# Optimization experiments

Hardware: AMD Instinct MI355X
Metric: run time of the kernel (lower is better)

The kernel has to match this reference:

```python
import jax, jax.numpy as jnp
import numpy as np

MIN_NORM = 1e-15
BALL_EPS = 4e-3          # float32 boundary eps (HGCN convention), c = 1
RES_LAMBDA = 0.5         # args.res_lambda (global in original repo)
N_HOPS = 2


def _artanh(x):
    x = jnp.clip(x, -1.0 + 1e-7, 1.0 - 1e-7)
    return 0.5 * jnp.log((1.0 + x) / (1.0 - x))


def _norm(x):
    return jnp.clip(jnp.linalg.norm(x, axis=-1, keepdims=True), MIN_NORM, None)


def expmap0(u):
    n = _norm(u)
    return jnp.tanh(n) * u / n


def mobius_add(x, y):
    x2 = jnp.sum(x * x, axis=-1, keepdims=True)
    y2 = jnp.sum(y * y, axis=-1, keepdims=True)
    xy = jnp.sum(x * y, axis=-1, keepdims=True)
    num = (1.0 + 2.0 * xy + y2) * x + (1.0 - x2) * y
    den = jnp.clip(1.0 + 2.0 * xy + x2 * y2, MIN_NORM, None)
    return num / den


def expmap(u, p):
    lam = 2.0 / jnp.clip(1.0 - jnp.sum(p * p, axis=-1, keepdims=True), MIN_NORM, None)
    n = _norm(u)
    second = jnp.tanh(0.5 * lam * n) * u / n
    return mobius_add(p, second)


def logmap(y, p):
    sub = mobius_add(-p, y)
    n = _norm(sub)
    lam = 2.0 / jnp.clip(1.0 - jnp.sum(p * p, axis=-1, keepdims=True), MIN_NORM, None)
    return (2.0 / lam) * _artanh(n) * sub / n


def project(x):
    n = _norm(x)
    maxnorm = 1.0 - BALL_EPS
    return jnp.where(n > maxnorm, x / n * maxnorm, x)


def _l2_normalize(x, eps=1e-12):
    return x / jnp.clip(jnp.linalg.norm(x, axis=-1, keepdims=True), eps, None)


def setup_inputs() -> dict:
    key = jax.random.key(0)
    k1, k2, k3, k4, k5 = jax.random.split(key, 5)
    n_entities, n_relations, latdim, n_edges = 200000, 32, 64, 1000000
    entity_emb = 0.1 * jax.random.normal(k1, (n_entities, latdim), dtype=jnp.float32)
    relation_emb = 0.1 * jax.random.normal(k2, (n_relations, latdim), dtype=jnp.float32)
    head = jax.random.randint(k3, (n_edges,), 0, n_entities)
    tail = jax.random.randint(k4, (n_edges,), 0, n_entities)
    edge_index = jnp.stack([head, tail], axis=0).astype(jnp.int64)
    edge_type = jax.random.randint(k5, (n_edges,), 1, n_relations + 1).astype(jnp.int64)
    return {"entity_emb": entity_emb, "relation_emb": relation_emb,
            "edge_index": edge_index, "edge_type": edge_type}


def _agg(entity_emb, relation_emb, head, tail, relation_type):
    n_entities = entity_emb.shape[0]
    head_emb = entity_emb[head]            # [E, d]
    tail_emb = entity_emb[tail]            # [E, d]
    rel_emb = relation_emb[relation_type]  # [E, d]
    ricci = _l2_normalize(tail_emb + rel_emb)
    hyper_head = expmap0(head_emb)
    hyper_tail = expmap(tail_emb, hyper_head)
    hyper_rel = expmap(rel_emb, hyper_head)
    res = project(mobius_add(hyper_tail, hyper_rel))
    res = logmap(res, hyper_head) + ricci * 1e-7
    res = jax.nn.relu(res)
    # scatter_mean by head index
    sums = jnp.zeros((n_entities, res.shape[-1]), res.dtype).at[head].add(res)
    counts = jnp.zeros((n_entities,), res.dtype).at[head].add(1.0)
    return sums / jnp.clip(counts, 1.0, None)[:, None]


def reference(entity_emb, relation_emb, edge_index, edge_type):
    head, tail = edge_index[0], edge_index[1]
    relation_type = edge_type - 1
    entity_res_emb = entity_emb
    e = entity_emb
    for _ in range(N_HOPS):
        e = _agg(e, relation_emb, head, tail, relation_type)
        e = _l2_normalize(e)  # F.normalize (dropout disabled for determinism)
        entity_res_emb = RES_LAMBDA * entity_res_emb + e
    return entity_res_emb
```

## Files before the change

### kernel.cpp

```cpp
#include <hip/hip_runtime.h>
#include <cmath>

#define MIN_NORM 1e-15f
#define RCPF(x)  __builtin_amdgcn_rcpf(x)
#define SQRTF(x) __builtin_amdgcn_sqrtf(x)
#define RSQF(x)  __builtin_amdgcn_rsqf(x)

template<int CTRL>
__device__ __forceinline__ float dpp_add(float v) {
    return __int_as_float(__builtin_amdgcn_update_dpp(0, __float_as_int(v), CTRL, 0xF, 0xF, false));
}

__device__ __forceinline__ float rsum16(float v) {
    v += dpp_add<0x121>(v);
    v += dpp_add<0x122>(v);
    v += dpp_add<0x124>(v);
    v += dpp_add<0x128>(v);
    return v;
}

__device__ __forceinline__ float rsum8(float v) {
    v += dpp_add<0xB1>(v);
    v += dpp_add<0x4E>(v);
    v += dpp_add<0x141>(v);
    return v;
}

__device__ __forceinline__ float tanh_fast(float x) {
    float ex = __expf(fminf(2.f * x, 30.f));
    return (ex - 1.f) * RCPF(ex + 1.f);
}

__global__ __launch_bounds__(256) void k_pass1(
    const int*    __restrict__ head,
    const float4* __restrict__ ent,
    const float4* __restrict__ rel,
    int*    __restrict__ C,
    float2* __restrict__ Th1,
    float2* __restrict__ Tt1,
    float2* __restrict__ RelC1,
    float2* __restrict__ RelC2,
    float ILAM2, int E, int N, int NR, int EB, int PG)
{
    int b = (int)blockIdx.x;
    if (b < EB) {
        int i = b * 256 + (int)threadIdx.x;
        if (i < E) atomicAdd(&C[head[i]], 1);
    } else if (b < EB + PG) {
        int gid = ((b - EB) * 256 + (int)threadIdx.x) >> 4;
        int g   = (int)threadIdx.x & 15;
        if (gid >= N) return;
        float4 v = ent[(size_t)gid * 16 + g];
        float n2 = rsum16(v.x * v.x + v.y * v.y + v.z * v.z + v.w * v.w);
        if (g == 0) {
            float nh     = fmaxf(SQRTF(fmaxf(n2, 0.f)), MIN_NORM);
            float inv_nh = RCPF(nh);
            float th     = tanh_fast(nh);
            Th1[gid] = make_float2(th * inv_nh, th * th);
            Tt1[gid] = make_float2(nh, inv_nh);
        }
    } else {
        int gid = ((b - EB - PG) * 256 + (int)threadIdx.x) >> 4;
        int g   = (int)threadIdx.x & 15;
        if (gid >= NR) return;
        float4 v = rel[(size_t)gid * 16 + g];
        float n2 = rsum16(v.x * v.x + v.y * v.y + v.z * v.z + v.w * v.w);
        if (g == 0) {
            float nr = fmaxf(SQRTF(n2), MIN_NORM);
            float inv_nr = RCPF(nr);
            RelC1[gid] = make_float2(nr, inv_nr);
            float thr2 = tanh_fast(ILAM2 * nr);
            RelC2[gid] = make_float2(thr2 * inv_nr, thr2 * thr2);
        }
    }
}

__global__ __launch_bounds__(256) void k_scan1(const int* __restrict__ C,
                                               int* __restrict__ T,
                                               int* __restrict__ BS,
                                               int* __restrict__ DH, int N) {
    __shared__ int lds[256];
    __shared__ int lh[64];
    if (threadIdx.x < 64) lh[threadIdx.x] = 0;
    int i = blockIdx.x * 256 + (int)threadIdx.x;
    int v = (i < N) ? C[i] : 0;
    lds[threadIdx.x] = v;
    __syncthreads();
    for (int off = 1; off < 256; off <<= 1) {
        int add = (threadIdx.x >= (unsigned)off) ? lds[threadIdx.x - off] : 0;
        __syncthreads();
        lds[threadIdx.x] += add;
        __syncthreads();
    }
    if (i < N) {
        T[i] = lds[threadIdx.x];
        int bd = 63 - min(v, 63);
        atomicAdd(&lh[bd], 1);
    }
    if (threadIdx.x == 255) BS[blockIdx.x] = lds[255];
    __syncthreads();
    if (threadIdx.x < 64 && lh[threadIdx.x] > 0)
        atomicAdd(&DH[threadIdx.x], lh[threadIdx.x]);
}

__global__ __launch_bounds__(1024) void k_scan2(int* __restrict__ BS,
                                                const int* __restrict__ DH,
                                                int* __restrict__ DB, int nb) {
    if (blockIdx.x == 0) {
        __shared__ int lds[1024];
        int v = ((int)threadIdx.x < nb) ? BS[threadIdx.x] : 0;
        lds[threadIdx.x] = v;
        __syncthreads();
        for (int off = 1; off < 1024; off <<= 1) {
            int add = (threadIdx.x >= (unsigned)off) ? lds[threadIdx.x - off] : 0;
            __syncthreads();
            lds[threadIdx.x] += add;
            __syncthreads();
        }
        if ((int)threadIdx.x < nb) BS[threadIdx.x] = lds[threadIdx.x] - v;
    } else {
        __shared__ int lds[64];
        if (threadIdx.x >= 64) return;
        int t = (int)threadIdx.x;
        int v = DH[t];
        lds[t] = v;
        __syncthreads();
        for (int off = 1; off < 64; off <<= 1) {
            int add = (t >= off) ? lds[t - off] : 0;
            __syncthreads();
            lds[t] += add;
            __syncthreads();
        }
        DB[t] = lds[t] - v;
    }
}

__global__ __launch_bounds__(256) void k_scan3(const int* __restrict__ C,
                                               const int* __restrict__ T,
                                               const int* __restrict__ BS,
                                               int2* __restrict__ OC,
                                               int* __restrict__ P, int N) {
    int i = blockIdx.x * 256 + (int)threadIdx.x;
    if (i < N) {
        int c = C[i];
        int beg = T[i] - c + BS[blockIdx.x];
        OC[i] = make_int2(beg, c);
        P[i] = beg;
    }
}

__global__ __launch_bounds__(256) void k_pass2(
    const int* __restrict__ C,
    int*       __restrict__ DB,
    int*       __restrict__ perm,
    const int* __restrict__ head,
    const int* __restrict__ tail,
    const int* __restrict__ etype,
    int*       __restrict__ P,
    int*       __restrict__ rec,
    int N, int E, int NB, int SLICES)
{
    int b = (int)blockIdx.x;
    if (b < NB) {
        __shared__ int lh[64];
        __shared__ int lbase[64];
        if (threadIdx.x < 64) lh[threadIdx.x] = 0;
        __syncthreads();
        int i = b * 256 + (int)threadIdx.x;
        int bd = -1, lr = 0;
        if (i < N) {
            bd = 63 - min(C[i], 63);
            lr = atomicAdd(&lh[bd], 1);
        }
        __syncthreads();
        if (threadIdx.x < 64 && lh[threadIdx.x] > 0)
            lbase[threadIdx.x] = atomicAdd(&DB[threadIdx.x], lh[threadIdx.x]);
        __syncthreads();
        if (bd >= 0) perm[lbase[bd] + lr] = i;
    } else {
        int region = b & 7;
        int slice  = (b - NB) >> 3;
        int rlo = (int)(((long long)region * N) >> 3);
        int rhi = (int)(((long long)(region + 1) * N) >> 3);
        int step = 256 * SLICES;
        for (int i = slice * 256 + (int)threadIdx.x; i < E; i += step) {
            int h = head[i];
            int t = tail[i];
            int et = etype[i];
            if (h >= rlo && h < rhi) {
                int pos = atomicAdd(&P[h], 1);
                rec[pos] = t | ((et - 1) << 20);
            }
        }
    }
}

template<bool HOP2>
__global__ __launch_bounds__(256) void rgat_hop_kernel(
    const float*  __restrict__ e,
    const float*  __restrict__ rel,
    const float2* __restrict__ Th1,
    const float2* __restrict__ Tt1,
    const float2* __restrict__ Tt2,
    const float2* __restrict__ RelC1,
    const float2* __restrict__ RelC2,
    const int*    __restrict__ rec,
    const int2*   __restrict__ OC,
    const int*    __restrict__ perm,
    const float*  __restrict__ ent,
    float*        __restrict__ dst0,
    float2*       __restrict__ Tt2w,
    float SCP2, float P2C, float ILAM2, int N)
{
    int tid  = blockIdx.x * 256 + (int)threadIdx.x;
    int slot = tid >> 3;
    int l    = (int)threadIdx.x & 7;
    bool act = slot < N;
    int h    = perm[act ? slot : 0];

    int2 oc = OC[h];
    int beg = act ? oc.x : 0;
    int end = act ? (oc.x + oc.y) : 0;

    const float* hrow = e + (size_t)h * 64 + l;
    float hv[8];
#pragma unroll
    for (int k = 0; k < 8; ++k) hv[k] = hrow[8 * k];

    float scp, p2;
    if constexpr (HOP2) {
        scp = SCP2; p2 = P2C;
    } else {
        float2 th = Th1[h];
        scp = th.x; p2 = th.y;
    }
    float bet  = fmaxf(1.f - p2, MIN_NORM);
    float ilam = RCPF(bet);
    float bet2 = bet * bet;

    float acc[8];
#pragma unroll
    for (int k = 0; k < 8; ++k) acc[k] = 0.f;

    float tA[8], rA[8], tB[8], rB[8];
    float2 tvA, rvA, tvB, rvB;

    auto LD = [&](int i, float* T, float* R, float2& TV, float2& RV) {
        int rc = rec[i];
        int ti = rc & 0xFFFFF;
        int ri = rc >> 20;
        const float* tr = e   + (size_t)ti * 64 + l;
        const float* rr = rel + (size_t)ri * 64 + l;
#pragma unroll
        for (int k = 0; k < 8; ++k) { T[k] = tr[8 * k]; R[k] = rr[8 * k]; }
        if constexpr (HOP2) { TV = Tt2[ti]; RV = RelC2[ri]; }
        else               { TV = Tt1[ti]; RV = RelC1[ri]; }
    };

    auto COMPUTE = [&](const float* t, const float* r, float2 tv, float2 rv) {
        float pht = 0.f, phr = 0.f, ptr_ = 0.f;
#pragma unroll
        for (int k = 0; k < 8; ++k) {
            pht  += hv[k] * t[k];
            phr  += hv[k] * r[k];
            ptr_ += t[k] * r[k];
        }
        float ht  = rsum8(pht);
        float hr  = rsum8(phr);
        float ttr = rsum8(ptr_);

        float sct, y2t, scr, y2r;
        if constexpr (HOP2) {
            sct = tv.x; y2t = tv.y;
            scr = rv.x; y2r = rv.y;
        } else {
            float tht = tanh_fast(ilam * tv.x);
            sct = tht * tv.y;  y2t = tht * tht;
            float thr_ = tanh_fast(ilam * rv.x);
            scr = thr_ * rv.y; y2r = thr_ * thr_;
        }

        float xyt = scp * sct * ht;
        float xyr = scp * scr * hr;

        float alt  = fmaf(2.f, xyt, 1.f + y2t);
        float dent = fmaxf(fmaf(p2, y2t, fmaf(2.f, xyt, 1.f)), MIN_NORM);
        float alr  = fmaf(2.f, xyr, 1.f + y2r);
        float denr = fmaxf(fmaf(p2, y2r, fmaf(2.f, xyr, 1.f)), MIN_NORM);
        float iS   = RCPF(dent * denr);
        float idt  = iS * denr;
        float idr  = iS * dent;

        float a2 = (alt * alt * p2 + 2.f * alt * bet * xyt + bet * bet * y2t) * idt * idt;
        float pa = fmaf(bet, xyt, alt * p2) * idt;
        float b2 = (alr * alr * p2 + 2.f * alr * bet * xyr + bet * bet * y2r) * idr * idr;
        float pb = fmaf(bet, xyr, alr * p2) * idr;

        float ytyr = sct * scr * ttr;
        float ab = (alt * alr * p2 + alt * bet * xyr + bet * alr * xyt + bet * bet * ytyr) * idt * idr;

        float am   = fmaf(2.f, ab, 1.f + b2);
        float bm   = 1.f - a2;
        float denm = fmaxf(fmaf(a2, b2, fmaf(2.f, ab, 1.f)), MIN_NORM);
        float idm  = RCPF(denm);
        float m2  = (am * am * a2 + 2.f * am * bm * ab + bm * bm * b2) * idm * idm;
        float pmv = fmaf(am, pa, bm * pb) * idm;

        const float maxn  = 1.f - 4e-3f;
        const float maxn2 = maxn * maxn;
        float irm = RSQF(fmaxf(m2, 1e-30f));
        float sc  = (m2 > maxn2) ? (maxn * irm) : 1.f;
        m2  *= sc * sc;
        pmv *= sc;

        float cs   = fmaf(-2.f, pmv, 1.f + m2);
        float dens = fmaxf(fmaf(p2, m2, fmaf(-2.f, pmv, 1.f)), MIN_NORM);
        float ids  = RCPF(dens);
        float s2  = fmaxf((cs * cs * p2 - 2.f * cs * bet * pmv + bet * bet * m2) * ids * ids, 1e-30f);
        float irs = RSQF(s2);
        float ns  = s2 * irs;
        float xa  = fminf(ns, 1.f - 1e-7f);
        float ath = 0.5f * __logf((1.f + xa) * RCPF(1.f - xa));
        float lgs = bet * ath * irs;

        float X  = am * idt;
        float Y  = bm * idr;
        float G  = idm * sc;
        float W  = lgs * ids;
        float WG = W * G;
        float Kt = WG * X * bet2 * sct;
        float Kr = WG * Y * bet2 * scr;
        float Z  = WG * bet * fmaf(X, alt, Y * alr);
        float Kh = scp * (Z - W * cs);

#pragma unroll
        for (int k = 0; k < 8; ++k)
            acc[k] += fmaxf(fmaf(Kh, hv[k], fmaf(Kt, t[k], Kr * r[k])), 0.f);
    };

    int i = beg;
    if (i < end) {
        LD(i, tA, rA, tvA, rvA);
        while (true) {
            if (i + 1 < end) LD(i + 1, tB, rB, tvB, rvB);
            COMPUTE(tA, rA, tvA, rvA);
            ++i;
            if (i >= end) break;
            if (i + 1 < end) LD(i + 1, tA, rA, tvA, rvA);
            COMPUTE(tB, rB, tvB, rvB);
            ++i;
            if (i >= end) break;
        }
    }

    if (!act) return;

    float pn = 0.f;
#pragma unroll
    for (int k = 0; k < 8; ++k) pn += acc[k] * acc[k];
    float n2 = rsum8(pn);
    float sn = SQRTF(n2);
    float inv = RCPF(fmaxf(sn, 1e-12f));

    float* dst = dst0 + (size_t)h * 64 + l;
    if constexpr (HOP2) {
        const float* en = ent + (size_t)h * 64 + l;
#pragma unroll
        for (int k = 0; k < 8; ++k)
            dst[8 * k] = fmaf(0.25f, en[8 * k], fmaf(0.5f, hv[k], acc[k] * inv));
    } else {
#pragma unroll
        for (int k = 0; k < 8; ++k) dst[8 * k] = acc[k] * inv;
        if (l == 0) {
            float nv = sn * inv;
            float nt = fmaxf(nv, MIN_NORM);
            float tht2 = tanh_fast(ILAM2 * nt);
            Tt2w[h] = make_float2(tht2 * RCPF(nt), tht2 * tht2);
        }
    }
}

extern "C" void kernel_launch(void* const* d_in, const int* in_sizes, int n_in,
                              void* d_out, int out_size, void* d_ws, size_t ws_size,
                              hipStream_t stream)
{
    const float* ent   = (const float*)d_in[0];
    const float* rel   = (const float*)d_in[1];
    const int*   eidx  = (const int*)d_in[2];
    const int*   etype = (const int*)d_in[3];

    int E = in_sizes[3];
    int N = in_sizes[0] / 64;
    int NR = in_sizes[1] / 64;
    const int* head = eidx;
    const int* tail = eidx + E;

    double th1d = tanh(1.0);
    float SCP2  = (float)th1d;
    float P2C   = (float)(th1d * th1d);
    float ILAM2 = (float)(1.0 / (1.0 - th1d * th1d));

    float*  A     = (float*)d_ws;
    int*    rec   = (int*)(A + (size_t)N * 64);
    int2*   OC    = (int2*)(rec + E);
    int*    P     = (int*)(OC + N);
    int*    C     = P + N;
    int*    DH    = C + N;
    int*    T     = DH + 64;
    int*    BS    = T + N;
    int*    DB    = BS + 1024;
    int*    perm  = DB + 64;
    float2* Th1   = (float2*)(perm + N);
    float2* Tt1   = Th1 + N;
    float2* Tt2   = Tt1 + N;
    float2* RelC1 = Tt2 + N;
    float2* RelC2 = RelC1 + NR;

    int NB = (N + 255) / 256;
    int EB = (E + 255) / 256;
    int PG = (N * 16 + 255) / 256;
    int RG = (NR * 16 + 255) / 256;
    const int SLICES = 104;

    float* out = (float*)d_out;
    dim3 blk(256);
    int hopGrid = (N * 8 + 255) / 256;

    (void)hipMemsetAsync(C, 0, (size_t)(N + 64) * sizeof(int), stream);

    k_pass1<<<EB + PG + RG, blk, 0, stream>>>(
        head, (const float4*)ent, (const float4*)rel,
        C, Th1, Tt1, RelC1, RelC2, ILAM2, E, N, NR, EB, PG);

    k_scan1<<<NB, blk, 0, stream>>>(C, T, BS, DH, N);
    k_scan2<<<2, 1024, 0, stream>>>(BS, DH, DB, NB);
    k_scan3<<<NB, blk, 0, stream>>>(C, T, BS, OC, P, N);

    k_pass2<<<NB + 8 * SLICES, blk, 0, stream>>>(
        C, DB, perm, head, tail, etype, P, rec, N, E, NB, SLICES);

    rgat_hop_kernel<false><<<hopGrid, blk, 0, stream>>>(
        ent, rel, Th1, Tt1, Tt2, RelC1, RelC2, rec, OC, perm,
        nullptr, A, Tt2, SCP2, P2C, ILAM2, N);

    rgat_hop_kernel<true><<<hopGrid, blk, 0, stream>>>(
        A, rel, Th1, Tt1, Tt2, RelC1, RelC2, rec, OC, perm,
        ent, out, nullptr, SCP2, P2C, ILAM2, N);
}
```

Baseline: 272.4 us.

## Store entity and relation embeddings as fp16 for hop gathers

Converts entity embeddings, relation embeddings and the hop-1 intermediate into half2 copies. Both hop kernels then gather from these copies, which halves the bytes read by the random gathers over about a million edges. Arithmetic stays in fp32 after conversion, and the final output is still written in fp32 using the original fp32 entity rows. The cost is fp16 rounding on the gathered embeddings and on the hop-1 result, which could affect accuracy, plus an extra conversion write in pass1.

```diff
diff --git a/kernel.cpp b/kernel.cpp
--- a/kernel.cpp
+++ b/kernel.cpp
@@ -1,4 +1,5 @@
 #include <hip/hip_runtime.h>
+#include <hip/hip_fp16.h>
 #include <cmath>
 
 #define MIN_NORM 1e-15f
@@ -35,11 +36,13 @@
     const int*    __restrict__ head,
     const float4* __restrict__ ent,
     const float4* __restrict__ rel,
-    int*    __restrict__ C,
-    float2* __restrict__ Th1,
-    float2* __restrict__ Tt1,
-    float2* __restrict__ RelC1,
-    float2* __restrict__ RelC2,
+    int*     __restrict__ C,
+    float2*  __restrict__ Th1,
+    float2*  __restrict__ Tt1,
+    float2*  __restrict__ RelC1,
+    float2*  __restrict__ RelC2,
+    __half2* __restrict__ EH2,
+    __half2* __restrict__ RelH2,
     float ILAM2, int E, int N, int NR, int EB, int PG)
 {
     int b = (int)blockIdx.x;
@@ -51,6 +54,8 @@
         int g   = (int)threadIdx.x & 15;
         if (gid >= N) return;
         float4 v = ent[(size_t)gid * 16 + g];
+        EH2[(size_t)gid * 32 + 2 * g]     = __floats2half2_rn(v.x, v.y);
+        EH2[(size_t)gid * 32 + 2 * g + 1] = __floats2half2_rn(v.z, v.w);
         float n2 = rsum16(v.x * v.x + v.y * v.y + v.z * v.z + v.w * v.w);
         if (g == 0) {
             float nh     = fmaxf(SQRTF(fmaxf(n2, 0.f)), MIN_NORM);
@@ -64,6 +69,8 @@
         int g   = (int)threadIdx.x & 15;
         if (gid >= NR) return;
         float4 v = rel[(size_t)gid * 16 + g];
+        RelH2[(size_t)gid * 32 + 2 * g]     = __floats2half2_rn(v.x, v.y);
+        RelH2[(size_t)gid * 32 + 2 * g + 1] = __floats2half2_rn(v.z, v.w);
         float n2 = rsum16(v.x * v.x + v.y * v.y + v.z * v.z + v.w * v.w);
         if (g == 0) {
             float nr = fmaxf(SQRTF(n2), MIN_NORM);
@@ -197,19 +204,20 @@
 
 template<bool HOP2>
 __global__ __launch_bounds__(256) void rgat_hop_kernel(
-    const float*  __restrict__ e,
-    const float*  __restrict__ rel,
-    const float2* __restrict__ Th1,
-    const float2* __restrict__ Tt1,
-    const float2* __restrict__ Tt2,
-    const float2* __restrict__ RelC1,
-    const float2* __restrict__ RelC2,
-    const int*    __restrict__ rec,
-    const int2*   __restrict__ OC,
-    const int*    __restrict__ perm,
-    const float*  __restrict__ ent,
-    float*        __restrict__ dst0,
-    float2*       __restrict__ Tt2w,
+    const __half2* __restrict__ e2,
+    const __half2* __restrict__ rel2,
+    const float2*  __restrict__ Th1,
+    const float2*  __restrict__ Tt1,
+    const float2*  __restrict__ Tt2,
+    const float2*  __restrict__ RelC1,
+    const float2*  __restrict__ RelC2,
+    const int*     __restrict__ rec,
+    const int2*    __restrict__ OC,
+    const int*     __restrict__ perm,
+    const float2*  __restrict__ entf2,
+    float2*        __restrict__ outf2,
+    __half2*       __restrict__ Ah2w,
+    float2*        __restrict__ Tt2w,
     float SCP2, float P2C, float ILAM2, int N)
 {
     int tid  = blockIdx.x * 256 + (int)threadIdx.x;
@@ -222,10 +230,13 @@
     int beg = act ? oc.x : 0;
     int end = act ? (oc.x + oc.y) : 0;
 
-    const float* hrow = e + (size_t)h * 64 + l;
+    const __half2* hrow = e2 + (size_t)h * 32 + l;
     float hv[8];
 #pragma unroll
-    for (int k = 0; k < 8; ++k) hv[k] = hrow[8 * k];
+    for (int k = 0; k < 4; ++k) {
+        float2 f = __half22float2(hrow[8 * k]);
+        hv[2 * k] = f.x; hv[2 * k + 1] = f.y;
+    }
 
     float scp, p2;
     if constexpr (HOP2) {
@@ -249,10 +260,15 @@
         int rc = rec[i];
         int ti = rc & 0xFFFFF;
         int ri = rc >> 20;
-        const float* tr = e   + (size_t)ti * 64 + l;
-        const float* rr = rel + (size_t)ri * 64 + l;
-#pragma unroll
-        for (int k = 0; k < 8; ++k) { T[k] = tr[8 * k]; R[k] = rr[8 * k]; }
+        const __half2* tr = e2   + (size_t)ti * 32 + l;
+        const __half2* rr = rel2 + (size_t)ri * 32 + l;
+#pragma unroll
+        for (int k = 0; k < 4; ++k) {
+            float2 ft = __half22float2(tr[8 * k]);
+            float2 fr = __half22float2(rr[8 * k]);
+            T[2 * k] = ft.x; T[2 * k + 1] = ft.y;
+            R[2 * k] = fr.x; R[2 * k + 1] = fr.y;
+        }
         if constexpr (HOP2) { TV = Tt2[ti]; RV = RelC2[ri]; }
         else               { TV = Tt1[ti]; RV = RelC1[ri]; }
     };
@@ -362,15 +378,22 @@
     float sn = SQRTF(n2);
     float inv = RCPF(fmaxf(sn, 1e-12f));
 
-    float* dst = dst0 + (size_t)h * 64 + l;
     if constexpr (HOP2) {
-        const float* en = ent + (size_t)h * 64 + l;
-#pragma unroll
-        for (int k = 0; k < 8; ++k)
-            dst[8 * k] = fmaf(0.25f, en[8 * k], fmaf(0.5f, hv[k], acc[k] * inv));
+        const float2* en = entf2 + (size_t)h * 32 + l;
+        float2*       dd = outf2 + (size_t)h * 32 + l;
+#pragma unroll
+        for (int k = 0; k < 4; ++k) {
+            float2 e = en[8 * k];
+            float2 o;
+            o.x = fmaf(0.25f, e.x, fmaf(0.5f, hv[2 * k],     acc[2 * k]     * inv));
+            o.y = fmaf(0.25f, e.y, fmaf(0.5f, hv[2 * k + 1], acc[2 * k + 1] * inv));
+            dd[8 * k] = o;
+        }
     } else {
-#pragma unroll
-        for (int k = 0; k < 8; ++k) dst[8 * k] = acc[k] * inv;
+        __half2* ad = Ah2w + (size_t)h * 32 + l;
+#pragma unroll
+        for (int k = 0; k < 4; ++k)
+            ad[8 * k] = __floats2half2_rn(acc[2 * k] * inv, acc[2 * k + 1] * inv);
         if (l == 0) {
             float nv = sn * inv;
             float nt = fmaxf(nv, MIN_NORM);
@@ -400,21 +423,23 @@
     float P2C   = (float)(th1d * th1d);
     float ILAM2 = (float)(1.0 / (1.0 - th1d * th1d));
 
-    float*  A     = (float*)d_ws;
-    int*    rec   = (int*)(A + (size_t)N * 64);
-    int2*   OC    = (int2*)(rec + E);
-    int*    P     = (int*)(OC + N);
-    int*    C     = P + N;
-    int*    DH    = C + N;
-    int*    T     = DH + 64;
-    int*    BS    = T + N;
-    int*    DB    = BS + 1024;
-    int*    perm  = DB + 64;
-    float2* Th1   = (float2*)(perm + N);
-    float2* Tt1   = Th1 + N;
-    float2* Tt2   = Tt1 + N;
-    float2* RelC1 = Tt2 + N;
-    float2* RelC2 = RelC1 + NR;
+    __half2* EH2   = (__half2*)d_ws;
+    __half2* Ah2   = EH2 + (size_t)N * 32;
+    __half2* RelH2 = Ah2 + (size_t)N * 32;
+    int*     rec   = (int*)(RelH2 + (size_t)NR * 32);
+    int2*    OC    = (int2*)(rec + E);
+    int*     P     = (int*)(OC + N);
+    int*     C     = P + N;
+    int*     DH    = C + N;
+    int*     T     = DH + 64;
+    int*     BS    = T + N;
+    int*     DB    = BS + 1024;
+    int*     perm  = DB + 64;
+    float2*  Th1   = (float2*)(perm + N);
+    float2*  Tt1   = Th1 + N;
+    float2*  Tt2   = Tt1 + N;
+    float2*  RelC1 = Tt2 + N;
+    float2*  RelC2 = RelC1 + NR;
 
     int NB = (N + 255) / 256;
     int EB = (E + 255) / 256;
@@ -430,7 +455,7 @@
 
     k_pass1<<<EB + PG + RG, blk, 0, stream>>>(
         head, (const float4*)ent, (const float4*)rel,
-        C, Th1, Tt1, RelC1, RelC2, ILAM2, E, N, NR, EB, PG);
+        C, Th1, Tt1, RelC1, RelC2, EH2, RelH2, ILAM2, E, N, NR, EB, PG);
 
     k_scan1<<<NB, blk, 0, stream>>>(C, T, BS, DH, N);
     k_scan2<<<2, 1024, 0, stream>>>(BS, DH, DB, NB);
@@ -440,10 +465,10 @@
         C, DB, perm, head, tail, etype, P, rec, N, E, NB, SLICES);
 
     rgat_hop_kernel<false><<<hopGrid, blk, 0, stream>>>(
-        ent, rel, Th1, Tt1, Tt2, RelC1, RelC2, rec, OC, perm,
-        nullptr, A, Tt2, SCP2, P2C, ILAM2, N);
+        EH2, RelH2, Th1, Tt1, Tt2, RelC1, RelC2, rec, OC, perm,
+        nullptr, nullptr, Ah2, Tt2, SCP2, P2C, ILAM2, N);
 
     rgat_hop_kernel<true><<<hopGrid, blk, 0, stream>>>(
-        A, rel, Th1, Tt1, Tt2, RelC1, RelC2, rec, OC, perm,
-        ent, out, nullptr, SCP2, P2C, ILAM2, N);
-}
+        Ah2, RelH2, Th1, Tt1, Tt2, RelC1, RelC2, rec, OC, perm,
+        (const float2*)ent, (float2*)out, nullptr, nullptr, SCP2, P2C, ILAM2, N);
+}
```

Result: faster. 258.4 us (-5.2%).
